# Kernel tuning notes

Measured on AMD Instinct MI355X. Metric: run time of the kernel, lower is better.

Reference implementation:

```python
import jax, jax.numpy as jnp
import numpy as np

D = 1024

def setup_inputs() -> dict:
    key = jax.random.key(0)
    ks = jax.random.split(key, 7)
    s = 1.0 / np.sqrt(D)
    return {
        "x": jax.random.normal(ks[0], (4, 2048, D), dtype=jnp.float32),
        "Wq": jax.random.uniform(ks[1], (D, D), jnp.float32, -s, s),
        "bq": jax.random.uniform(ks[2], (D,), jnp.float32, -s, s),
        "Wk": jax.random.uniform(ks[3], (D, D), jnp.float32, -s, s),
        "bk": jax.random.uniform(ks[4], (D,), jnp.float32, -s, s),
        "Wv": jax.random.uniform(ks[5], (D, D), jnp.float32, -s, s),
        "bv": jax.random.uniform(ks[6], (D,), jnp.float32, -s, s),
    }

def reference(x, Wq, bq, Wk, bk, Wv, bv):
    # x: [b, s, d]; Linear layers: y = x @ W^T + b (torch convention)
    q = jnp.einsum('bsd,ed->bse', x, Wq) + bq
    k = jnp.einsum('bsd,ed->bse', x, Wk) + bk
    v = jnp.einsum('bsd,ed->bse', x, Wv) + bv
    # NOTE: original module does NOT scale by 1/sqrt(d)
    scores = jnp.einsum('bqd,bkd->bqk', q, k)  # [b, s, s]
    attn = jax.nn.softmax(scores, axis=-1)
    return jnp.einsum('bqk,bkd->bqd', attn, v)
```

## Files before the change

kernel.cpp:

```cpp
#include <hip/hip_runtime.h>

typedef _Float16 half8 __attribute__((ext_vector_type(8)));
typedef float floatx4 __attribute__((ext_vector_type(4)));

__device__ __forceinline__ void gld_lds16(const void* g, void* l) {
  __builtin_amdgcn_global_load_lds(
      (const __attribute__((address_space(1))) void*)g,
      (__attribute__((address_space(3))) void*)l, 16, 0, 0);
}

#define SB() __builtin_amdgcn_sched_barrier(0)
#define LGKM(n) asm volatile("s_waitcnt lgkmcnt(" #n ")" ::: "memory")
#define VMC0() asm volatile("s_waitcnt vmcnt(0)" ::: "memory")
#define BAR() __builtin_amdgcn_s_barrier()
#define PRIO1() __builtin_amdgcn_s_setprio(1)
#define PRIO0() __builtin_amdgcn_s_setprio(0)

template <int MODE>
__global__ __launch_bounds__(256, 2) void gemmd(
    const _Float16* __restrict__ Ag, const _Float16* __restrict__ Bg,
    void* __restrict__ Cg, const float* __restrict__ bcat) {
  constexpr int KS   = MODE == 0 ? 1024 : (MODE == 1 ? 3072 : 2048);
  constexpr int NK   = MODE == 2 ? 32 : 16;
  constexpr int NWG  = MODE == 0 ? 1536 : (MODE == 1 ? 1024 : 512);
  constexpr int CSTR = MODE == 0 ? 3072 : (MODE == 1 ? 2048 : 1024);

  int g = (int)blockIdx.x;
  g = (g & 7) * (NWG / 8) + (g >> 3);

  int row0, col0;
  const _Float16 *Ap, *Bp;
  _Float16* C16 = nullptr;
  float* C32 = nullptr;
  if constexpr (MODE == 0) {
    const int tm = g / 24, tn = g % 24;
    row0 = tm * 128; col0 = tn * 128;
    Ap = Ag + (size_t)row0 * 1024;
    Bp = Bg + (size_t)col0 * 1024;
    C16 = (_Float16*)Cg;
  } else if constexpr (MODE == 1) {
    const int z = g >> 8, r = g & 255, tm = r >> 4, tn = r & 15;
    row0 = tm * 128; col0 = tn * 128;
    Ap = Ag + (size_t)z * 6291456 + (size_t)row0 * 3072;
    Bp = Ag + (size_t)z * 6291456 + (size_t)col0 * 3072 + 1024;
    C16 = (_Float16*)Cg + (size_t)z * 4194304;
  } else {
    const int z = g >> 7, r = g & 127, tm = r >> 3, tn = r & 7;
    row0 = tm * 128; col0 = tn * 128;
    Ap = Ag + (size_t)z * 4194304 + (size_t)row0 * 2048;
    Bp = Bg + (size_t)z * 2097152 + (size_t)col0 * 2048;
    C32 = (float*)Cg + (size_t)z * 2097152;
  }

  __shared__ _Float16 lds[32768];
  const int tid = threadIdx.x, lane = tid & 63, wid = tid >> 6;
  const int wm = wid >> 1, wn = wid & 1;
  const int wrow = wm * 64, wcol = wn * 64;
  const int fr = lane & 15, u = lane >> 4, w7 = lane & 7;
  const int k0e = ((u ^ w7) << 3), k1e = (((4 + u) ^ w7) << 3);
  const int srow = tid >> 3;
  const int sgl = (((tid & 7) ^ (srow & 7)) << 3);

  floatx4 acc[4][4] = {};
  half8 aF[8], bF[8];

  auto stage1 = [&](const _Float16* Gp, int rowoff, int kt, int dst) {
    gld_lds16(Gp + (size_t)(rowoff + srow) * KS + kt + sgl, &lds[dst + tid * 8]);
  };
  auto stageT = [&](int kt, int p) {
#pragma unroll
    for (int c = 0; c < 4; ++c) stage1(Ap, c * 32, kt, p * 8192 + c * 2048);
#pragma unroll
    for (int c = 0; c < 4; ++c) stage1(Bp, c * 32, kt, 16384 + p * 8192 + c * 2048);
  };
  auto ldA4 = [&](int p) {
#pragma unroll
    for (int mf = 0; mf < 4; ++mf) {
      const int ro = p * 8192 + (wrow + mf * 16 + fr) * 64;
      aF[mf * 2 + 0] = *(const half8*)&lds[ro + k0e];
      aF[mf * 2 + 1] = *(const half8*)&lds[ro + k1e];
    }
  };
  auto ldB2 = [&](int p, int nf0) {
#pragma unroll
    for (int nf = 0; nf < 2; ++nf) {
      const int ro = 16384 + p * 8192 + (wcol + (nf0 + nf) * 16 + fr) * 64;
      bF[(nf0 + nf) * 2 + 0] = *(const half8*)&lds[ro + k0e];
      bF[(nf0 + nf) * 2 + 1] = *(const half8*)&lds[ro + k1e];
    }
  };
  auto burst = [&](int nf0) {
#pragma unroll
    for (int mf = 0; mf < 4; ++mf)
#pragma unroll
      for (int nf = 0; nf < 2; ++nf)
#pragma unroll
        for (int kk = 0; kk < 2; ++kk)
          acc[mf][nf0 + nf] = __builtin_amdgcn_mfma_f32_16x16x32_f16(
              aF[mf * 2 + kk], bF[(nf0 + nf) * 2 + kk], acc[mf][nf0 + nf], 0, 0, 0);
  };

  stageT(0, 0);
  VMC0();
  BAR();

#pragma unroll 1
  for (int t = 0; t < NK; ++t) {
    const int p = t & 1;
    if (t + 1 < NK) stageT(t * 64 + 64, p ^ 1);
    SB();
    ldA4(p); SB(); ldB2(p, 0); SB(); ldB2(p, 2); SB();
    LGKM(4); SB(); PRIO1(); burst(0); PRIO0(); SB();
    LGKM(0); SB(); PRIO1(); burst(2); PRIO0(); SB();
    if (t + 1 < NK) VMC0();
    BAR();
  }

  const int r0 = row0 + wrow + u * 4;
  const int c0 = col0 + wcol + fr;
#pragma unroll
  for (int mf = 0; mf < 4; ++mf)
#pragma unroll
    for (int nf = 0; nf < 4; ++nf) {
      const int col = c0 + nf * 16;
      float badd = 0.f;
      if constexpr (MODE == 0) badd = bcat[col];
#pragma unroll
      for (int j = 0; j < 4; ++j) {
        const int row = r0 + mf * 16 + j;
        if constexpr (MODE == 2)
          C32[(size_t)row * CSTR + col] = acc[mf][nf][j];
        else
          C16[(size_t)row * CSTR + col] = (_Float16)(acc[mf][nf][j] + badd);
      }
    }
}

__global__ __launch_bounds__(256) void prep(
    const float* __restrict__ x, const float* __restrict__ wq,
    const float* __restrict__ wk, const float* __restrict__ wv,
    const float* __restrict__ bq, const float* __restrict__ bk,
    const float* __restrict__ bv, _Float16* __restrict__ x16,
    _Float16* __restrict__ W16, float* __restrict__ bcat) {
  const int b = blockIdx.x, t = threadIdx.x;
  auto cv8 = [](const float* src, _Float16* dst) {
    const float4* p = (const float4*)src;
    float4 a = p[0], bb = p[1];
    half8 h;
    h[0] = (_Float16)a.x; h[1] = (_Float16)a.y; h[2] = (_Float16)a.z; h[3] = (_Float16)a.w;
    h[4] = (_Float16)bb.x; h[5] = (_Float16)bb.y; h[6] = (_Float16)bb.z; h[7] = (_Float16)bb.w;
    *(half8*)dst = h;
  };
  if (b < 2048) {
    const int i = b * 256 + t;
#pragma unroll
    for (int c = 0; c < 2; ++c) {
      const size_t j = (size_t)(i + c * 524288) * 8;
      cv8(x + j, x16 + j);
    }
  } else if (b < 3584) {
    const int idx = (b - 2048) * 256 + t;
    const int m = idx >> 17, j = idx & 131071;
    const float* src = m == 0 ? wq : (m == 1 ? wk : wv);
    cv8(src + (size_t)j * 8, W16 + (size_t)m * 1048576 + (size_t)j * 8);
  } else {
    const int i = (b - 3584) * 256 + t;
    const float* s = i < 1024 ? bq : (i < 2048 ? bk : bv);
    bcat[i] = s[i & 1023];
  }
}

__global__ __launch_bounds__(256) void transpose_v(const _Float16* __restrict__ QKV,
                                                   _Float16* __restrict__ Vt) {
  __shared__ _Float16 t[32][36];
  const int b = blockIdx.z;
  const int e0 = blockIdx.x * 32;
  const int s0 = blockIdx.y * 32;
  const int tid = threadIdx.x;
  const int r = tid >> 3;
  const int c4 = (tid & 7) * 4;
  const _Float16* src = QKV + (size_t)(b * 2048 + s0 + r) * 3072 + 2048 + e0 + c4;
#pragma unroll
  for (int j = 0; j < 4; ++j) t[r][c4 + j] = src[j];
  __syncthreads();
  _Float16* dst = Vt + ((size_t)b * 1024 + e0 + r) * 2048 + s0 + c4;
#pragma unroll
  for (int j = 0; j < 4; ++j) dst[j] = t[c4 + j][r];
}

__global__ __launch_bounds__(256) void softmax_rows_f16(_Float16* __restrict__ S) {
  __shared__ float red[4];
  _Float16* s = S + (size_t)blockIdx.x * 2048;
  const int tid = threadIdx.x;
  float v[8];
  {
    half8 h = *(const half8*)(s + tid * 8);
#pragma unroll
    for (int j = 0; j < 8; ++j) v[j] = (float)h[j];
  }
  float m = v[0];
#pragma unroll
  for (int j = 1; j < 8; ++j) m = fmaxf(m, v[j]);
#pragma unroll
  for (int off = 32; off > 0; off >>= 1) m = fmaxf(m, __shfl_xor(m, off));
  if ((tid & 63) == 0) red[tid >> 6] = m;
  __syncthreads();
  m = fmaxf(fmaxf(red[0], red[1]), fmaxf(red[2], red[3]));
  float sum = 0.f;
#pragma unroll
  for (int j = 0; j < 8; ++j) { v[j] = __expf(v[j] - m); sum += v[j]; }
#pragma unroll
  for (int off = 32; off > 0; off >>= 1) sum += __shfl_xor(sum, off);
  __syncthreads();
  if ((tid & 63) == 0) red[tid >> 6] = sum;
  __syncthreads();
  sum = red[0] + red[1] + red[2] + red[3];
  const float inv = 1.0f / sum;
  half8 h;
#pragma unroll
  for (int j = 0; j < 8; ++j) h[j] = (_Float16)(v[j] * inv);
  *(half8*)(s + tid * 8) = h;
}

extern "C" void kernel_launch(void* const* d_in, const int* in_sizes, int n_in,
                              void* d_out, int out_size, void* d_ws, size_t ws_size,
                              hipStream_t stream) {
  (void)in_sizes; (void)n_in; (void)out_size;
  const float* x  = (const float*)d_in[0];
  const float* Wq = (const float*)d_in[1];
  const float* bq = (const float*)d_in[2];
  const float* Wk = (const float*)d_in[3];
  const float* bk = (const float*)d_in[4];
  const float* Wv = (const float*)d_in[5];
  const float* bv = (const float*)d_in[6];
  float* out = (float*)d_out;

  char* ws = (char*)d_ws;
  size_t off = 0;
  auto alloc = [&](size_t bytes) {
    char* p = ws + off;
    off += (bytes + 255) & ~255ull;
    return p;
  };
  _Float16* x16  = (_Float16*)alloc(8192ull * 1024 * 2);
  _Float16* W16  = (_Float16*)alloc(3072ull * 1024 * 2);
  _Float16* QKV  = (_Float16*)alloc(8192ull * 3072 * 2);
  _Float16* Vt   = (_Float16*)alloc(4096ull * 1024 * 4);
  _Float16* Sc   = (_Float16*)alloc(4ull * 2048 * 2048 * 2);
  float*    bcat = (float*)alloc(3072 * 4);
  if (off > ws_size) return;

  prep<<<3596, 256, 0, stream>>>(x, Wq, Wk, Wv, bq, bk, bv, x16, W16, bcat);

  gemmd<0><<<1536, 256, 0, stream>>>(x16, W16, QKV, bcat);
  transpose_v<<<dim3(32, 64, 4), 256, 0, stream>>>(QKV, Vt);

  gemmd<1><<<1024, 256, 0, stream>>>(QKV, QKV, Sc, nullptr);
  softmax_rows_f16<<<8192, 256, 0, stream>>>(Sc);
  gemmd<2><<<512, 256, 0, stream>>>(Sc, Vt, out, nullptr);
}
```

Before: 158.8 us.

## Replace QK^T GEMM with 256x256-tile 8-wave kernel using interleaved staging

The scores GEMM (Q·K^T) moves from the generic 128x128-tile, 4-wave kernel to a dedicated 256x256-tile kernel with 512 threads and 8 waves, 128 KB of LDS, and double-buffered A/B tiles. Global-to-LDS loads for the next A tile and the tile after next for B are interleaved between four MFMA quadrant bursts with partial vmcnt waits, instead of waiting for all loads each iteration. Larger tiles halve global/L2 traffic per FLOP but give only 256 workgroups and low occupancy. The many barriers and hand-tuned wait counts add risk of stalls or races.

```diff
diff --git a/kernel.cpp b/kernel.cpp
--- a/kernel.cpp
+++ b/kernel.cpp
@@ -11,19 +11,116 @@
 
 #define SB() __builtin_amdgcn_sched_barrier(0)
 #define LGKM(n) asm volatile("s_waitcnt lgkmcnt(" #n ")" ::: "memory")
-#define VMC0() asm volatile("s_waitcnt vmcnt(0)" ::: "memory")
+#define VMC(n) asm volatile("s_waitcnt vmcnt(" #n ")" ::: "memory")
 #define BAR() __builtin_amdgcn_s_barrier()
 #define PRIO1() __builtin_amdgcn_s_setprio(1)
 #define PRIO0() __builtin_amdgcn_s_setprio(0)
+
+__global__ __launch_bounds__(512, 2) void gemm8x(const _Float16* __restrict__ QKV,
+                                                 _Float16* __restrict__ Sc) {
+  int g = (int)blockIdx.x;
+  g = (g & 7) * 32 + (g >> 3);
+  const int z = g >> 6, r = g & 63, tm = r >> 3, tn = r & 7;
+  const int row0 = tm * 256, col0 = tn * 256;
+  const _Float16* Ap = QKV + ((size_t)z * 2048 + row0) * 3072;
+  const _Float16* Bp = QKV + ((size_t)z * 2048 + col0) * 3072 + 1024;
+  _Float16* C16 = Sc + (size_t)z * 4194304;
+
+  __shared__ _Float16 lds[65536];
+  const int tid = threadIdx.x, lane = tid & 63, wid = tid >> 6;
+  const int wm = wid >> 2, wn = wid & 3;
+  const int fr = lane & 15, u = lane >> 4, w7 = lane & 7;
+  const int k0e = ((u ^ w7) << 3), k1e = (((4 + u) ^ w7) << 3);
+  const int srow = tid >> 3;
+  const int sgl = (((tid & 7) ^ (srow & 7)) << 3);
+
+  floatx4 acc[8][4] = {};
+  half8 aF[8], bF0[4], bF1[4];
+
+  auto stg = [&](const _Float16* Gp, int rowoff, int kt, int dst) {
+    gld_lds16(Gp + (size_t)(rowoff + srow) * 3072 + kt + sgl, &lds[dst + tid * 8]);
+  };
+  auto stA = [&](int kt, int p, int h) {
+    stg(Ap, h * 128, kt, p * 16384 + h * 8192);
+    stg(Ap, h * 128 + 64, kt, p * 16384 + h * 8192 + 4096);
+  };
+  auto stB = [&](int kt, int p, int h) {
+    stg(Bp, h * 128, kt, 32768 + p * 16384 + h * 8192);
+    stg(Bp, h * 128 + 64, kt, 32768 + p * 16384 + h * 8192 + 4096);
+  };
+  auto ldA = [&](int p, int mh) {
+#pragma unroll
+    for (int mf = 0; mf < 4; ++mf) {
+      const int ro = p * 16384 + (wm * 128 + mh * 64 + mf * 16 + fr) * 64;
+      aF[mf * 2 + 0] = *(const half8*)&lds[ro + k0e];
+      aF[mf * 2 + 1] = *(const half8*)&lds[ro + k1e];
+    }
+  };
+  auto ldB = [&](int p, int nh, half8* bF) {
+#pragma unroll
+    for (int nf = 0; nf < 2; ++nf) {
+      const int ro = 32768 + p * 16384 + (wn * 64 + nh * 32 + nf * 16 + fr) * 64;
+      bF[nf * 2 + 0] = *(const half8*)&lds[ro + k0e];
+      bF[nf * 2 + 1] = *(const half8*)&lds[ro + k1e];
+    }
+  };
+  auto Q = [&](int mh, int nh, half8* bF) {
+#pragma unroll
+    for (int mf = 0; mf < 4; ++mf)
+#pragma unroll
+      for (int nf = 0; nf < 2; ++nf)
+#pragma unroll
+        for (int kk = 0; kk < 2; ++kk)
+          acc[mh * 4 + mf][nh * 2 + nf] = __builtin_amdgcn_mfma_f32_16x16x32_f16(
+              aF[mf * 2 + kk], bF[nf * 2 + kk], acc[mh * 4 + mf][nh * 2 + nf], 0, 0, 0);
+  };
+
+  stA(0, 0, 0); stA(0, 0, 1); stB(0, 0, 0); stB(0, 0, 1);
+  stB(64, 1, 0); stB(64, 1, 1);
+  VMC(4); BAR();
+
+  constexpr int NK = 16;
+#pragma unroll 1
+  for (int t = 0; t < NK; ++t) {
+    const int p = t & 1, kt = t * 64;
+    ldA(p, 0); SB(); ldB(p, 0, bF0); SB();
+    if (t + 1 < NK) stA(kt + 64, p ^ 1, 0);
+    SB(); LGKM(8); SB();
+    BAR(); LGKM(0); SB(); PRIO1(); Q(0, 0, bF0); PRIO0(); SB(); BAR();
+    ldB(p, 1, bF1); SB();
+    if (t + 1 < NK) stA(kt + 64, p ^ 1, 1);
+    SB();
+    BAR(); LGKM(0); SB(); PRIO1(); Q(0, 1, bF1); PRIO0(); SB(); VMC(8); BAR();
+    ldA(p, 1); SB();
+    if (t + 2 < NK) stB(kt + 128, p, 0);
+    SB();
+    BAR(); LGKM(0); SB(); PRIO1(); Q(1, 0, bF0); PRIO0(); SB(); BAR();
+    if (t + 2 < NK) stB(kt + 128, p, 1);
+    SB();
+    BAR(); PRIO1(); Q(1, 1, bF1); PRIO0(); SB();
+    if (t + 2 < NK) { VMC(6); } else if (t + 1 < NK) { VMC(0); }
+    BAR();
+  }
+
+  const int r0 = row0 + wm * 128 + u * 4;
+  const int c0 = col0 + wn * 64 + fr;
+#pragma unroll
+  for (int mf = 0; mf < 8; ++mf)
+#pragma unroll
+    for (int nf = 0; nf < 4; ++nf)
+#pragma unroll
+      for (int j = 0; j < 4; ++j)
+        C16[(size_t)(r0 + mf * 16 + j) * 2048 + c0 + nf * 16] = (_Float16)acc[mf][nf][j];
+}
 
 template <int MODE>
 __global__ __launch_bounds__(256, 2) void gemmd(
     const _Float16* __restrict__ Ag, const _Float16* __restrict__ Bg,
     void* __restrict__ Cg, const float* __restrict__ bcat) {
-  constexpr int KS   = MODE == 0 ? 1024 : (MODE == 1 ? 3072 : 2048);
+  constexpr int KS   = MODE == 0 ? 1024 : 2048;
   constexpr int NK   = MODE == 2 ? 32 : 16;
-  constexpr int NWG  = MODE == 0 ? 1536 : (MODE == 1 ? 1024 : 512);
-  constexpr int CSTR = MODE == 0 ? 3072 : (MODE == 1 ? 2048 : 1024);
+  constexpr int NWG  = MODE == 0 ? 1536 : 512;
+  constexpr int CSTR = MODE == 0 ? 3072 : 1024;
 
   int g = (int)blockIdx.x;
   g = (g & 7) * (NWG / 8) + (g >> 3);
@@ -38,12 +135,6 @@
     Ap = Ag + (size_t)row0 * 1024;
     Bp = Bg + (size_t)col0 * 1024;
     C16 = (_Float16*)Cg;
-  } else if constexpr (MODE == 1) {
-    const int z = g >> 8, r = g & 255, tm = r >> 4, tn = r & 15;
-    row0 = tm * 128; col0 = tn * 128;
-    Ap = Ag + (size_t)z * 6291456 + (size_t)row0 * 3072;
-    Bp = Ag + (size_t)z * 6291456 + (size_t)col0 * 3072 + 1024;
-    C16 = (_Float16*)Cg + (size_t)z * 4194304;
   } else {
     const int z = g >> 7, r = g & 127, tm = r >> 3, tn = r & 7;
     row0 = tm * 128; col0 = tn * 128;
@@ -101,7 +192,7 @@
   };
 
   stageT(0, 0);
-  VMC0();
+  VMC(0);
   BAR();
 
 #pragma unroll 1
@@ -112,7 +203,7 @@
     ldA4(p); SB(); ldB2(p, 0); SB(); ldB2(p, 2); SB();
     LGKM(4); SB(); PRIO1(); burst(0); PRIO0(); SB();
     LGKM(0); SB(); PRIO1(); burst(2); PRIO0(); SB();
-    if (t + 1 < NK) VMC0();
+    if (t + 1 < NK) VMC(0);
     BAR();
   }
 
@@ -255,7 +346,7 @@
   gemmd<0><<<1536, 256, 0, stream>>>(x16, W16, QKV, bcat);
   transpose_v<<<dim3(32, 64, 4), 256, 0, stream>>>(QKV, Vt);
 
-  gemmd<1><<<1024, 256, 0, stream>>>(QKV, QKV, Sc, nullptr);
+  gemm8x<<<256, 512, 0, stream>>>(QKV, Sc);
   softmax_rows_f16<<<8192, 256, 0, stream>>>(Sc);
   gemmd<2><<<512, 256, 0, stream>>>(Sc, Vt, out, nullptr);
 }
```

Measured after the change: 158.8 us, median of 2. About the same (-0.0%).
